# Performance work log

Hardware: AMD Instinct MI355X
Metric: run time of the kernel (lower is better)

The kernel has to match this reference:

```python
import jax, jax.numpy as jnp
import numpy as np

B, D, H, K = 8192, 1280, 16384, 64


def setup_inputs() -> dict:
    key = jax.random.key(0)
    k1, k2, k3 = jax.random.split(key, 3)
    x = jax.random.normal(k1, (B, D), dtype=jnp.float32)
    # encoder weight [hidden_dim, input_dim] (torch Linear layout)
    W_enc = jax.random.normal(k2, (H, D), dtype=jnp.float32) * (1.0 / np.sqrt(D))
    b_enc = jnp.zeros((H,), dtype=jnp.float32)
    # decoder weight [input_dim, hidden_dim], unit-norm columns scaled by 0.1
    W_dec = jax.random.normal(k3, (D, H), dtype=jnp.float32)
    W_dec = 0.1 * W_dec / jnp.linalg.norm(W_dec, axis=0, keepdims=True)
    b_dec = jnp.zeros((D,), dtype=jnp.float32)
    b_pre = jnp.zeros((D,), dtype=jnp.float32)
    return {"x": x, "W_enc": W_enc, "b_enc": b_enc, "W_dec": W_dec,
            "b_dec": b_dec, "b_pre": b_pre, "k": K}


def reference(x, W_enc, b_enc, W_dec, b_dec, b_pre, k):
    # --- encode ---
    x_centered = x - b_pre                                   # [B, D]
    pre = jnp.einsum('bd,hd->bh', x_centered, W_enc) + b_enc  # [B, H]
    vals, idx = jax.lax.top_k(pre, k)                        # [B, k]
    rows = jnp.arange(pre.shape[0])[:, None]                 # [B, 1]
    hidden = jnp.zeros_like(pre).at[rows, idx].set(jax.nn.relu(vals))  # [B, H]
    # --- decode ---
    reconstructed = jnp.einsum('bh,dh->bd', hidden, W_dec) + b_dec + b_pre
    # --- losses ---
    reconstruction_loss = jnp.mean((reconstructed - x) ** 2)
    l0 = jnp.mean(jnp.sum((hidden > 0).astype(jnp.float32), axis=-1))
    sparsity_loss = jnp.array(0.0, dtype=jnp.float32)
    loss = reconstruction_loss
    return reconstructed, hidden, loss, reconstruction_loss, sparsity_loss, l0
```

## Files before the change

### kernel.cpp

```cpp
#include <hip/hip_runtime.h>
#include <hip/hip_bf16.h>

constexpr int K_MAX    = 128;
constexpr int S_MAX    = 128;
constexpr int A_MAX    = 256;
constexpr int CAND_MAX = 512;
constexpr int BM = 128, BN = 128, BKF = 16;
constexpr int NBITER = 42;
constexpr int D_MAX   = 2048;
constexpr int H_FIX   = 16384;

typedef __attribute__((ext_vector_type(8))) short bf16x8;
typedef __attribute__((ext_vector_type(8))) unsigned short u16x8;
typedef __attribute__((ext_vector_type(4))) float f32x4;

__device__ inline unsigned short f2bf(float f) {
  unsigned u = __float_as_uint(f);
  return (unsigned short)((u + 0x7fff + ((u >> 16) & 1)) >> 16);
}
__device__ inline unsigned short key_of(float f) {
  unsigned short b = f2bf(f);
  return b ^ ((b & 0x8000) ? 0xFFFF : 0x8000);
}
__device__ inline float val_of_key(unsigned short kk) {
  unsigned short b = (kk & 0x8000) ? (unsigned short)(kk ^ 0x8000)
                                   : (unsigned short)(kk ^ 0xFFFF);
  return __uint_as_float(((unsigned)b) << 16);
}
__device__ inline float bf2f(unsigned short b) {
  return __uint_as_float(((unsigned)b) << 16);
}

__device__ inline int lds_slot(int r, int c) {
  return ((r >> 1) << 4) | ((r & 1) << 3) | (c ^ ((r >> 1) & 7));
}

__global__ __launch_bounds__(256) void prep_xb(
    const float* __restrict__ x, const float* __restrict__ b_pre,
    unsigned short* __restrict__ Xb, int D, size_t total4)
{
  for (size_t i = blockIdx.x * 256 + threadIdx.x; i < total4; i += (size_t)gridDim.x * 256) {
    const size_t e = i * 4;
    const int d = (int)(e % D);
    float4 xv = *reinterpret_cast<const float4*>(x + e);
    float4 bp = *reinterpret_cast<const float4*>(b_pre + d);
    ushort4 o;
    o.x = f2bf(xv.x - bp.x); o.y = f2bf(xv.y - bp.y);
    o.z = f2bf(xv.z - bp.z); o.w = f2bf(xv.w - bp.w);
    *reinterpret_cast<ushort4*>(Xb + e) = o;
  }
}

__global__ __launch_bounds__(256) void prep_wb(
    const float* __restrict__ W, unsigned short* __restrict__ Wb, size_t total4)
{
  for (size_t i = blockIdx.x * 256 + threadIdx.x; i < total4; i += (size_t)gridDim.x * 256) {
    const size_t e = i * 4;
    float4 wv = *reinterpret_cast<const float4*>(W + e);
    ushort4 o;
    o.x = f2bf(wv.x); o.y = f2bf(wv.y); o.z = f2bf(wv.z); o.w = f2bf(wv.w);
    *reinterpret_cast<ushort4*>(Wb + e) = o;
  }
}

__global__ __launch_bounds__(256) void enc_gemm_bf16(
    const unsigned short* __restrict__ Xb, const unsigned short* __restrict__ Wb,
    const float* __restrict__ b_enc, float* __restrict__ pre, int D, int H)
{
  __shared__ unsigned short As[2][128 * 64];
  __shared__ unsigned short Bs[2][128 * 64];
  const int tid  = threadIdx.x;
  const int wave = tid >> 6, lane = tid & 63;

  int lin = blockIdx.y * gridDim.x + blockIdx.x;
  const int nwg = gridDim.x * gridDim.y;
  if ((nwg & 7) == 0) {
    const int cpx = nwg >> 3;
    lin = (lin & 7) * cpx + (lin >> 3);
  }
  const int m0 = (lin / gridDim.x) * 128, n0 = (lin % gridDim.x) * 128;

  const int wm = (wave >> 1) * 64, wn = (wave & 1) * 64;
  const int l16 = lane & 15, lhi = lane >> 4;

  f32x4 acc[4][4];
#pragma unroll
  for (int i = 0; i < 4; ++i)
#pragma unroll
    for (int j = 0; j < 4; ++j) acc[i][j] = (f32x4){0.f, 0.f, 0.f, 0.f};

  const int NT = D / 64;

#pragma unroll
  for (int i = 0; i < 4; ++i) {
    const int base = wave * 64 + i * 256;
    const int idx  = base + lane;
    const int sr = idx >> 4, u = idx & 15;
    const int row = (sr << 1) | (u >> 3);
    const int ch  = (u & 7) ^ (sr & 7);
    __builtin_amdgcn_global_load_lds(
        (const __attribute__((address_space(1))) unsigned int*)(Xb + (size_t)(m0 + row) * D + ch * 8),
        (__attribute__((address_space(3))) unsigned int*)(As[0] + (size_t)base * 8), 16, 0, 0);
    __builtin_amdgcn_global_load_lds(
        (const __attribute__((address_space(1))) unsigned int*)(Wb + (size_t)(n0 + row) * D + ch * 8),
        (__attribute__((address_space(3))) unsigned int*)(Bs[0] + (size_t)base * 8), 16, 0, 0);
  }
  __syncthreads();

  int cur = 0;
  for (int t = 0; t < NT; ++t) {
    if (t + 1 < NT) {
      const int kb = (t + 1) * 64;
      const int nxt = cur ^ 1;
#pragma unroll
      for (int i = 0; i < 4; ++i) {
        const int base = wave * 64 + i * 256;
        const int idx  = base + lane;
        const int sr = idx >> 4, u = idx & 15;
        const int row = (sr << 1) | (u >> 3);
        const int ch  = (u & 7) ^ (sr & 7);
        __builtin_amdgcn_global_load_lds(
            (const __attribute__((address_space(1))) unsigned int*)(Xb + (size_t)(m0 + row) * D + kb + ch * 8),
            (__attribute__((address_space(3))) unsigned int*)(As[nxt] + (size_t)base * 8), 16, 0, 0);
        __builtin_amdgcn_global_load_lds(
            (const __attribute__((address_space(1))) unsigned int*)(Wb + (size_t)(n0 + row) * D + kb + ch * 8),
            (__attribute__((address_space(3))) unsigned int*)(Bs[nxt] + (size_t)base * 8), 16, 0, 0);
      }
    }
#pragma unroll
    for (int kk = 0; kk < 2; ++kk) {
      bf16x8 af[4], bfr[4];
#pragma unroll
      for (int mi = 0; mi < 4; ++mi)
        af[mi] = *reinterpret_cast<const bf16x8*>(
            As[cur] + (size_t)lds_slot(wm + mi * 16 + l16, kk * 4 + lhi) * 8);
#pragma unroll
      for (int ni = 0; ni < 4; ++ni)
        bfr[ni] = *reinterpret_cast<const bf16x8*>(
            Bs[cur] + (size_t)lds_slot(wn + ni * 16 + l16, kk * 4 + lhi) * 8);
#pragma unroll
      for (int mi = 0; mi < 4; ++mi)
#pragma unroll
        for (int ni = 0; ni < 4; ++ni)
          acc[mi][ni] = __builtin_amdgcn_mfma_f32_16x16x32_bf16(af[mi], bfr[ni], acc[mi][ni], 0, 0, 0);
    }
    __syncthreads();
    cur ^= 1;
  }

#pragma unroll
  for (int ni = 0; ni < 4; ++ni) {
    const int n = n0 + wn + ni * 16 + l16;
    const float be = b_enc[n];
#pragma unroll
    for (int mi = 0; mi < 4; ++mi) {
      const int mbase = m0 + wm + mi * 16 + lhi * 4;
#pragma unroll
      for (int r = 0; r < 4; ++r) {
        unsigned short* prow = (unsigned short*)(pre + (size_t)(mbase + r) * H);
        prow[n] = key_of(acc[mi][ni][r] + be);
      }
    }
  }
}

__global__ __launch_bounds__(256) void topk_classify_keys(
    const float* __restrict__ hidden,
    int* __restrict__ sure_ix, float* __restrict__ sure_val, int* __restrict__ sure_cnt,
    int* __restrict__ amb_ix, int* __restrict__ amb_cnt,
    const int* __restrict__ kptr, float delta)
{
  constexpr int H = H_FIX, NC = H_FIX / (256 * 8);
  __shared__ int hist[4096];
  __shared__ int chunk[256];
  __shared__ int misc[8];

  const int tid = threadIdx.x, b = blockIdx.x;
  const int k = min(*kptr, K_MAX);
  const unsigned short* krow = (const unsigned short*)(hidden + (size_t)b * H);

  if (tid < 8) misc[tid] = 0;
  for (int i = tid; i < 4096; i += 256) hist[i] = 0;

  u16x8 kv[NC];
#pragma unroll
  for (int i = 0; i < NC; ++i)
    kv[i] = *reinterpret_cast<const u16x8*>(krow + ((size_t)i * 256 + tid) * 8);
  __syncthreads();

#pragma unroll
  for (int i = 0; i < NC; ++i)
#pragma unroll
    for (int j = 0; j < 8; ++j)
      atomicAdd(&hist[((unsigned)(unsigned short)kv[i][j]) >> 4], 1);
  __syncthreads();

  int csum = 0;
#pragma unroll
  for (int j = 0; j < 16; ++j) csum += hist[tid * 16 + j];
  chunk[tid] = csum;
  __syncthreads();
  int gt = 0;
  for (int j = tid + 1; j < 256; ++j) gt += chunk[j];
  {
    int run = gt;
#pragma unroll
    for (int j = 15; j >= 0; --j) {
      const int hc = hist[tid * 16 + j];
      if (run < k && k <= run + hc) { misc[0] = tid * 16 + j; misc[1] = run; }
      run += hc;
    }
  }
  __syncthreads();
  const int b1 = misc[0];
  if (tid < 16) chunk[tid] = 0;
  __syncthreads();
#pragma unroll
  for (int i = 0; i < NC; ++i)
#pragma unroll
    for (int j = 0; j < 8; ++j) {
      const unsigned kk = (unsigned)(unsigned short)kv[i][j];
      if ((int)(kk >> 4) == b1) atomicAdd(&chunk[kk & 15], 1);
    }
  __syncthreads();
  if (tid == 0) {
    int run = misc[1];
    int K16 = b1 << 4;
    for (int j = 15; j >= 0; --j) {
      const int c = chunk[j];
      if (run < k && k <= run + c) K16 = (b1 << 4) | j;
      run += c;
    }
    const float v_lo = val_of_key((unsigned short)K16);
    const float v_hi = val_of_key((unsigned short)min(K16 + 1, 65535));
    const float ulp = v_hi - v_lo;
    const float vs = v_hi + delta;
    const float va = v_lo - ulp - delta;
    int ks = key_of(vs); if (val_of_key((unsigned short)ks) > vs) --ks;
    int ka = key_of(va); if (val_of_key((unsigned short)ka) < va) ++ka;
    misc[2] = ks; misc[3] = ka;
  }
  __syncthreads();
  const unsigned ks = (unsigned)misc[2], ka = (unsigned)misc[3];

#pragma unroll
  for (int i = 0; i < NC; ++i)
#pragma unroll
    for (int j = 0; j < 8; ++j) {
      const unsigned kk = (unsigned)(unsigned short)kv[i][j];
      if (kk > ks) {
        const int p = atomicAdd(&misc[4], 1);
        if (p < S_MAX) {
          const int h = (i * 256 + tid) * 8 + j;
          sure_ix[(size_t)b * S_MAX + p] = h;
          sure_val[(size_t)b * S_MAX + p] = val_of_key((unsigned short)kk);
        }
      } else if (kk >= ka) {
        const int p = atomicAdd(&misc[5], 1);
        if (p < A_MAX) amb_ix[(size_t)b * A_MAX + p] = (i * 256 + tid) * 8 + j;
      }
    }
  __syncthreads();
  if (tid == 0) {
    sure_cnt[b] = min(misc[4], S_MAX);
    amb_cnt[b]  = min(misc[5], A_MAX);
  }
}

__global__ __launch_bounds__(256) void refine_f64(
    const float* __restrict__ X, const float* __restrict__ b_pre,
    const float* __restrict__ W, const float* __restrict__ b_enc,
    const int* __restrict__ amb_ix, const int* __restrict__ amb_cnt,
    double* __restrict__ amb_sv, int D)
{
  __shared__ float xr[D_MAX];
  const int tid = threadIdx.x, b = blockIdx.x;
  const int C = min(amb_cnt[b], A_MAX);
  for (int d = tid; d < D; d += 256) xr[d] = X[(size_t)b * D + d] - b_pre[d];
  __syncthreads();
  const int wid = tid >> 6, lane = tid & 63;
  for (int c = wid; c < C; c += 4) {
    const int h = amb_ix[(size_t)b * A_MAX + c];
    const float* wr = W + (size_t)h * D;
    double s0 = 0.0, s1 = 0.0;
    int i = lane;
    for (; i + 64 < D; i += 128) {
      s0 += (double)xr[i] * (double)wr[i];
      s1 += (double)xr[i + 64] * (double)wr[i + 64];
    }
    if (i < D) s0 += (double)xr[i] * (double)wr[i];
    double s = s0 + s1;
    for (int off = 32; off; off >>= 1) s += __shfl_xor(s, off);
    if (lane == 0) amb_sv[(size_t)b * A_MAX + c] = s + (double)b_enc[h];
  }
}

__global__ __launch_bounds__(256) void rank_scatter2(
    const int* __restrict__ sure_ix, const float* __restrict__ sure_val,
    const int* __restrict__ sure_cnt,
    const int* __restrict__ amb_ix, const double* __restrict__ amb_sv,
    const int* __restrict__ amb_cnt, const int* __restrict__ kptr,
    float* __restrict__ hidden, int* __restrict__ tk_idx, float* __restrict__ tk_val)
{
  constexpr int H = H_FIX;
  __shared__ double asv[A_MAX];
  __shared__ int    aix[A_MAX];
  const int tid = threadIdx.x, b = blockIdx.x;
  const int k = min(*kptr, K_MAX);
  const int S = min(min(sure_cnt[b], S_MAX), k);
  const int A = min(amb_cnt[b], A_MAX);
  float* hrow = hidden + (size_t)b * H;

  for (int c = tid; c < A; c += 256) {
    asv[c] = amb_sv[(size_t)b * A_MAX + c];
    aix[c] = amb_ix[(size_t)b * A_MAX + c];
  }
  const float4 z4 = {0.f, 0.f, 0.f, 0.f};
  for (int i = tid; i < (H >> 2); i += 256)
    reinterpret_cast<float4*>(hrow)[i] = z4;
  __syncthreads();

  for (int i = tid; i < S; i += 256) {
    const int h = sure_ix[(size_t)b * S_MAX + i];
    const float v = sure_val[(size_t)b * S_MAX + i];
    const float rv = (v > 0.f) ? v : 0.f;
    hrow[h] = rv;
    tk_idx[(size_t)b * K_MAX + i] = h;
    tk_val[(size_t)b * K_MAX + i] = rv;
  }
  const int m = k - S;
  for (int c = tid; c < A; c += 256) {
    const double v = asv[c];
    const int h = aix[c];
    int r = 0;
    for (int j = 0; j < A; ++j) {
      const double vj = asv[j];
      r += ((vj > v) || (vj == v && aix[j] < h)) ? 1 : 0;
    }
    if (r < m) {
      const float rv = (v > 0.0) ? (float)v : 0.f;
      hrow[h] = rv;
      tk_idx[(size_t)b * K_MAX + S + r] = h;
      tk_val[(size_t)b * K_MAX + S + r] = rv;
    }
  }
}

__global__ __launch_bounds__(256, 2) void topk_select(
    const float* __restrict__ X, const float* __restrict__ b_pre,
    const float* __restrict__ W, const float* __restrict__ b_enc,
    float* __restrict__ hidden, int* __restrict__ tk_idx, float* __restrict__ tk_val,
    const int* __restrict__ kptr, int D, float margin)
{
  constexpr int H = H_FIX, NC = H_FIX / (256 * 8);
  __shared__ double cand_sv[CAND_MAX];
  __shared__ float  xr[D_MAX];
  __shared__ int    cand_ix[CAND_MAX];
  __shared__ int    hist[4096];
  __shared__ int    chunk[256];
  __shared__ int    misc[8];

  const int tid = threadIdx.x, b = blockIdx.x;
  const int k = min(*kptr, K_MAX);
  float* hrow = hidden + (size_t)b * H;
  const unsigned short* krow = (const unsigned short*)hrow;

  if (tid < 8) misc[tid] = 0;
  for (int i = tid; i < 4096; i += 256) hist[i] = 0;
  for (int d = tid; d < D; d += 256) xr[d] = X[(size_t)b * D + d] - b_pre[d];

  u16x8 kv[NC];
#pragma unroll
  for (int i = 0; i < NC; ++i)
    kv[i] = *reinterpret_cast<const u16x8*>(krow + ((size_t)i * 256 + tid) * 8);
  __syncthreads();

#pragma unroll
  for (int i = 0; i < NC; ++i)
#pragma unroll
    for (int j = 0; j < 8; ++j)
      atomicAdd(&hist[((unsigned)(unsigned short)kv[i][j]) >> 4], 1);
  __syncthreads();

  int csum = 0;
#pragma unroll
  for (int j = 0; j < 16; ++j) csum += hist[tid * 16 + j];
  chunk[tid] = csum;
  __syncthreads();
  int gt = 0;
  for (int j = tid + 1; j < 256; ++j) gt += chunk[j];
  {
    int run = gt;
#pragma unroll
    for (int j = 15; j >= 0; --j) {
      const int hc = hist[tid * 16 + j];
      if (run < k && k <= run + hc) { misc[0] = tid * 16 + j; misc[1] = run; }
      run += hc;
    }
  }
  __syncthreads();
  const int b1 = misc[0];
  if (tid < 16) chunk[tid] = 0;
  __syncthreads();
#pragma unroll
  for (int i = 0; i < NC; ++i)
#pragma unroll
    for (int j = 0; j < 8; ++j) {
      const unsigned kk = (unsigned)(unsigned short)kv[i][j];
      if ((int)(kk >> 4) == b1) atomicAdd(&chunk[kk & 15], 1);
    }
  __syncthreads();
  if (tid == 0) {
    int run = misc[1];
    int K16 = b1 << 4;
    for (int j = 15; j >= 0; --j) {
      const int c = chunk[j];
      if (run < k && k <= run + c) K16 = (b1 << 4) | j;
      run += c;
    }
    const float vthr = val_of_key((unsigned short)K16) - margin;
    int kt = (int)key_of(vthr);
    if (kt > K16) kt = K16;
    misc[2] = kt;
  }
  __syncthreads();
  const unsigned kthr = (unsigned)misc[2];

#pragma unroll
  for (int i = 0; i < NC; ++i)
#pragma unroll
    for (int j = 0; j < 8; ++j) {
      if ((unsigned)(unsigned short)kv[i][j] >= kthr) {
        const int pos = atomicAdd(&misc[3], 1);
        if (pos < CAND_MAX) cand_ix[pos] = (i * 256 + tid) * 8 + j;
      }
    }
  __syncthreads();
  const int C = min(misc[3], CAND_MAX);

  const float4 z4 = {0.f, 0.f, 0.f, 0.f};
  for (int i = tid; i < (H >> 2); i += 256)
    reinterpret_cast<float4*>(hrow)[i] = z4;

  const int wid = tid >> 6, lane = tid & 63;
  for (int c = wid; c < C; c += 4) {
    const int h = cand_ix[c];
    const float* wr = W + (size_t)h * D;
    double s = 0.0;
    for (int i = lane; i < D; i += 64) s += (double)xr[i] * (double)wr[i];
    for (int off = 32; off; off >>= 1) s += __shfl_xor(s, off);
    if (lane == 0) cand_sv[c] = s + (double)b_enc[h];
  }
  __syncthreads();

  for (int c = tid; c < C; c += 256) {
    const double v = cand_sv[c];
    const int h = cand_ix[c];
    int r = 0;
    for (int j = 0; j < C; ++j) {
      const double vj = cand_sv[j];
      r += ((vj > v) || (vj == v && cand_ix[j] < h)) ? 1 : 0;
    }
    if (r < k) {
      const float rv = (v > 0.0) ? (float)v : 0.f;
      hrow[h] = rv;
      tk_idx[(size_t)b * K_MAX + r] = h;
      tk_val[(size_t)b * K_MAX + r] = rv;
    }
  }
}

__global__ __launch_bounds__(256) void enc_gemm_f32(
    const float* __restrict__ X, const float* __restrict__ W,
    const float* __restrict__ b_enc, const float* __restrict__ b_pre,
    float* __restrict__ pre, int D, int H)
{
  __shared__ float As[BKF][BM + 4];
  __shared__ float Bs[BKF][BN + 4];
  const int tid = threadIdx.x;
  const int m0 = blockIdx.y * BM;
  const int n0 = blockIdx.x * BN;
  const int tx = tid & 15, ty = tid >> 4;
  float acc[8][8];
#pragma unroll
  for (int i = 0; i < 8; ++i)
#pragma unroll
    for (int j = 0; j < 8; ++j) acc[i][j] = 0.f;

  for (int kb = 0; kb < D; kb += BKF) {
#pragma unroll
    for (int t = 0; t < 2; ++t) {
      const int f4i = tid + t * 256;
      const int row = f4i >> 2;
      const int kq  = (f4i & 3) << 2;
      float4 xv = *reinterpret_cast<const float4*>(X + (size_t)(m0 + row) * D + kb + kq);
      float4 bp = *reinterpret_cast<const float4*>(b_pre + kb + kq);
      As[kq + 0][row] = xv.x - bp.x; As[kq + 1][row] = xv.y - bp.y;
      As[kq + 2][row] = xv.z - bp.z; As[kq + 3][row] = xv.w - bp.w;
      float4 wv = *reinterpret_cast<const float4*>(W + (size_t)(n0 + row) * D + kb + kq);
      Bs[kq + 0][row] = wv.x; Bs[kq + 1][row] = wv.y;
      Bs[kq + 2][row] = wv.z; Bs[kq + 3][row] = wv.w;
    }
    __syncthreads();
#pragma unroll
    for (int kk = 0; kk < BKF; ++kk) {
      float4 a0 = *reinterpret_cast<const float4*>(&As[kk][ty * 8]);
      float4 a1 = *reinterpret_cast<const float4*>(&As[kk][ty * 8 + 4]);
      float4 b0 = *reinterpret_cast<const float4*>(&Bs[kk][tx * 8]);
      float4 b1 = *reinterpret_cast<const float4*>(&Bs[kk][tx * 8 + 4]);
      float av[8] = {a0.x, a0.y, a0.z, a0.w, a1.x, a1.y, a1.z, a1.w};
      float bv[8] = {b0.x, b0.y, b0.z, b0.w, b1.x, b1.y, b1.z, b1.w};
#pragma unroll
      for (int i = 0; i < 8; ++i)
#pragma unroll
        for (int j = 0; j < 8; ++j) acc[i][j] += av[i] * bv[j];
    }
    __syncthreads();
  }
#pragma unroll
  for (int i = 0; i < 8; ++i) {
    const size_t m = (size_t)(m0 + ty * 8 + i);
#pragma unroll
    for (int j = 0; j < 8; j += 4) {
      const int n = n0 + tx * 8 + j;
      float4 o;
      o.x = acc[i][j + 0] + b_enc[n + 0];
      o.y = acc[i][j + 1] + b_enc[n + 1];
      o.z = acc[i][j + 2] + b_enc[n + 2];
      o.w = acc[i][j + 3] + b_enc[n + 3];
      *reinterpret_cast<float4*>(pre + m * H + n) = o;
    }
  }
}

__global__ __launch_bounds__(256) void topk_refine(
    const float* __restrict__ X, const float* __restrict__ b_pre,
    const float* __restrict__ W, const float* __restrict__ b_enc,
    float* __restrict__ hidden, int* __restrict__ tk_idx, float* __restrict__ tk_val,
    const int* __restrict__ kptr, int D, int H, float margin)
{
  extern __shared__ char smem_raw[];
  double* cand_val = reinterpret_cast<double*>(smem_raw);
  float*  xr       = reinterpret_cast<float*>(cand_val + CAND_MAX);
  int*    cand_idx = reinterpret_cast<int*>(xr + D);
  int*    misc     = cand_idx + CAND_MAX;

  const int tid = threadIdx.x;
  const int b = blockIdx.x;
  const int k = min(*kptr, K_MAX);
  float* hrow = hidden + (size_t)b * H;

  for (int i = tid; i < NBITER + 2; i += 256) misc[i] = 0;
  for (int d = tid; d < D; d += 256) xr[d] = X[(size_t)b * D + d] - b_pre[d];

  float f[64];
#pragma unroll
  for (int i = 0; i < 16; ++i) {
    const int base = i * 1024 + tid * 4;
    float4 v = {-3e38f, -3e38f, -3e38f, -3e38f};
    if (base + 3 < H) v = *reinterpret_cast<const float4*>(hrow + base);
    f[4 * i + 0] = v.x; f[4 * i + 1] = v.y; f[4 * i + 2] = v.z; f[4 * i + 3] = v.w;
  }
  __syncthreads();

  float lo = -1e4f, hi = 1e4f;
  for (int it = 0; it < NBITER; ++it) {
    const float mid = 0.5f * (lo + hi);
    int cnt = 0;
#pragma unroll
    for (int j = 0; j < 64; ++j) cnt += (f[j] >= mid) ? 1 : 0;
    for (int off = 32; off; off >>= 1) cnt += __shfl_xor(cnt, off);
    if ((tid & 63) == 0) atomicAdd(&misc[it], cnt);
    __syncthreads();
    if (misc[it] >= k) lo = mid; else hi = mid;
  }

  const float thresh = lo - margin;
#pragma unroll
  for (int j = 0; j < 64; ++j) {
    if (f[j] >= thresh) {
      const int h = (j >> 2) * 1024 + tid * 4 + (j & 3);
      if (h < H) {
        int pos = atomicAdd(&misc[NBITER], 1);
        if (pos < CAND_MAX) cand_idx[pos] = h;
      }
    }
  }
  __syncthreads();
  const int C = min(misc[NBITER], CAND_MAX);

  const int wid = tid >> 6, lane = tid & 63;
  for (int c = wid; c < C; c += 4) {
    const int h = cand_idx[c];
    const float* wr = W + (size_t)h * D;
    double s = 0.0;
    for (int i = lane; i < D; i += 64) s += (double)xr[i] * (double)wr[i];
    for (int off = 32; off; off >>= 1) s += __shfl_xor(s, off);
    if (lane == 0) cand_val[c] = s + (double)b_enc[h];
  }
  __syncthreads();

  const float4 z4 = {0.f, 0.f, 0.f, 0.f};
  for (int i = tid; i < (H >> 2); i += 256)
    reinterpret_cast<float4*>(hrow)[i] = z4;
  __syncthreads();

  for (int c = tid; c < C; c += 256) {
    const double v = cand_val[c];
    const int h = cand_idx[c];
    int r = 0;
    for (int j = 0; j < C; ++j) {
      const double vj = cand_val[j];
      r += ((vj > v) || (vj == v && cand_idx[j] < h)) ? 1 : 0;
    }
    if (r < k) {
      const float rv = (v > 0.0) ? (float)v : 0.f;
      hrow[h] = rv;
      tk_idx[(size_t)b * K_MAX + r] = h;
      tk_val[(size_t)b * K_MAX + r] = rv;
    }
  }
}

__global__ __launch_bounds__(256) void transpose_wdec_bf16(
    const float* __restrict__ Wsrc, unsigned short* __restrict__ WT, int D, int H)
{
  __shared__ float tile[32][33];
  const int c  = threadIdx.x & 31;
  const int r0 = threadIdx.x >> 5;
  const int h0 = blockIdx.x * 32;
  const int d0 = blockIdx.y * 32;
#pragma unroll
  for (int r = r0; r < 32; r += 8) {
    const int d = d0 + r, h = h0 + c;
    if (d < D && h < H) tile[r][c] = Wsrc[(size_t)d * H + h];
  }
  __syncthreads();
#pragma unroll
  for (int r = r0; r < 32; r += 8) {
    const int h = h0 + r, d = d0 + c;
    if (h < H && d < D) WT[(size_t)h * D + d] = f2bf(tile[c][r]);
  }
}

__global__ __launch_bounds__(256) void decode_loss(
    const float* __restrict__ X, const float* __restrict__ b_pre,
    const float* __restrict__ b_dec, const float* __restrict__ Wfull,
    const unsigned short* __restrict__ WTb,
    const int* __restrict__ tk_idx, const float* __restrict__ tk_val,
    const int* __restrict__ kptr,
    float* __restrict__ recon, double* __restrict__ row_ssq,
    int D, int H, int useWT)
{
  __shared__ int   sidx[K_MAX];
  __shared__ float sval[K_MAX];
  __shared__ double sd[4];
  const int tid = threadIdx.x, b = blockIdx.x;
  const int k = min(*kptr, K_MAX);
  if (tid < k) {
    sidx[tid] = tk_idx[(size_t)b * K_MAX + tid];
    sval[tid] = tk_val[(size_t)b * K_MAX + tid];
  }
  __syncthreads();
  double ssq = 0.0;
  const int D4 = D >> 2;
  for (int dc = tid; dc < D4; dc += 256) {
    const int d = dc * 4;
    float4 bd = *reinterpret_cast<const float4*>(b_dec + d);
    float4 bp = *reinterpret_cast<const float4*>(b_pre + d);
    float4 a = {bd.x + bp.x, bd.y + bp.y, bd.z + bp.z, bd.w + bp.w};
    if (useWT) {
#pragma unroll 4
      for (int j = 0; j < k; ++j) {
        const ushort4 w = *reinterpret_cast<const ushort4*>(WTb + (size_t)sidx[j] * D + d);
        const float s = sval[j];
        a.x += s * bf2f(w.x); a.y += s * bf2f(w.y);
        a.z += s * bf2f(w.z); a.w += s * bf2f(w.w);
      }
    } else {
#pragma unroll 4
      for (int j = 0; j < k; ++j) {
        const float s = sval[j];
        const int h = sidx[j];
        a.x += s * Wfull[(size_t)(d + 0) * H + h];
        a.y += s * Wfull[(size_t)(d + 1) * H + h];
        a.z += s * Wfull[(size_t)(d + 2) * H + h];
        a.w += s * Wfull[(size_t)(d + 3) * H + h];
      }
    }
    *reinterpret_cast<float4*>(recon + (size_t)b * D + d) = a;
    float4 xv = *reinterpret_cast<const float4*>(X + (size_t)b * D + d);
    const double d0 = (double)a.x - (double)xv.x;
    const double d1 = (double)a.y - (double)xv.y;
    const double d2 = (double)a.z - (double)xv.z;
    const double d3 = (double)a.w - (double)xv.w;
    ssq += d0 * d0 + d1 * d1 + d2 * d2 + d3 * d3;
  }
  for (int off = 32; off; off >>= 1) ssq += __shfl_xor(ssq, off);
  if ((tid & 63) == 0) sd[tid >> 6] = ssq;
  __syncthreads();
  if (tid == 0) row_ssq[b] = sd[0] + sd[1] + sd[2] + sd[3];
}

__global__ __launch_bounds__(256) void finalize_part(
    const double* __restrict__ row_ssq, const float* __restrict__ tk_val,
    const int* __restrict__ kptr, double* __restrict__ part_s, int* __restrict__ part_c,
    int Bdim, int rows_per_blk)
{
  __shared__ double sd[4];
  __shared__ int si[4];
  const int tid = threadIdx.x;
  const int k = min(*kptr, K_MAX);
  const int b0 = blockIdx.x * rows_per_blk;
  const int b1 = min(b0 + rows_per_blk, Bdim);
  double s = 0.0;
  for (int i = b0 + tid; i < b1; i += 256) s += row_ssq[i];
  int cnt = 0;
  const int total = (b1 - b0) * k;
  for (int i = tid; i < total; i += 256) {
    const int bb = b0 + i / k, j = i - (i / k) * k;
    cnt += (tk_val[(size_t)bb * K_MAX + j] > 0.f) ? 1 : 0;
  }
  for (int off = 32; off; off >>= 1) { s += __shfl_xor(s, off); cnt += __shfl_xor(cnt, off); }
  if ((tid & 63) == 0) { sd[tid >> 6] = s; si[tid >> 6] = cnt; }
  __syncthreads();
  if (tid == 0) {
    part_s[blockIdx.x] = sd[0] + sd[1] + sd[2] + sd[3];
    part_c[blockIdx.x] = si[0] + si[1] + si[2] + si[3];
  }
}

__global__ __launch_bounds__(64) void finalize_k2(
    const double* __restrict__ part_s, const int* __restrict__ part_c,
    float* __restrict__ scalars, int nparts, int Bdim, int D)
{
  const int tid = threadIdx.x;
  double s = (tid < nparts) ? part_s[tid] : 0.0;
  int cnt = (tid < nparts) ? part_c[tid] : 0;
  for (int off = 32; off; off >>= 1) { s += __shfl_xor(s, off); cnt += __shfl_xor(cnt, off); }
  if (tid == 0) {
    const double rl = s / ((double)Bdim * (double)D);
    scalars[0] = (float)rl;
    scalars[1] = (float)rl;
    scalars[2] = 0.f;
    scalars[3] = (float)((double)cnt / Bdim);
  }
}

extern "C" void kernel_launch(void* const* d_in, const int* in_sizes, int n_in,
                              void* d_out, int out_size, void* d_ws, size_t ws_size,
                              hipStream_t stream)
{
  const float* x     = (const float*)d_in[0];
  const float* W_enc = (const float*)d_in[1];
  const float* b_enc = (const float*)d_in[2];
  const float* W_dec = (const float*)d_in[3];
  const float* b_dec = (const float*)d_in[4];
  const float* b_pre = (const float*)d_in[5];
  const int*   kptr  = (const int*)d_in[6];

  const int D = in_sizes[4];
  const int H = in_sizes[2];
  const int B = in_sizes[0] / D;

  float* recon   = (float*)d_out;
  float* hidden  = recon + (size_t)B * D;
  float* scalars = hidden + (size_t)B * H;

  size_t off = 0;
  int* tk_idx = (int*)((char*)d_ws + off);        off += (size_t)B * K_MAX * sizeof(int);
  float* tk_val = (float*)((char*)d_ws + off);    off += (size_t)B * K_MAX * sizeof(float);
  off = (off + 7) & ~(size_t)7;
  double* row_ssq = (double*)((char*)d_ws + off); off += (size_t)B * sizeof(double);
  double* part_s = (double*)((char*)d_ws + off);  off += 64 * sizeof(double);
  int* part_c = (int*)((char*)d_ws + off);        off += 64 * sizeof(int);
  off = (off + 7) & ~(size_t)7;

  unsigned short* Xb = (unsigned short*)((char*)d_ws + off);
  off += (size_t)B * D * sizeof(unsigned short);
  unsigned short* Wb = (unsigned short*)((char*)d_ws + off);
  off += (size_t)H * D * sizeof(unsigned short);
  const int useBF16 = (off <= ws_size) ? 1 : 0;

  unsigned short* WTb = (unsigned short*)((char*)d_ws + off);
  off += (size_t)D * H * sizeof(unsigned short);
  const int useWT = (off <= ws_size) ? 1 : 0;

  int* sure_ix = (int*)((char*)d_ws + off);       off += (size_t)B * S_MAX * sizeof(int);
  float* sure_val = (float*)((char*)d_ws + off);  off += (size_t)B * S_MAX * sizeof(float);
  int* sure_cnt = (int*)((char*)d_ws + off);      off += (size_t)B * sizeof(int);
  int* amb_ix = (int*)((char*)d_ws + off);        off += (size_t)B * A_MAX * sizeof(int);
  int* amb_cnt = (int*)((char*)d_ws + off);       off += (size_t)B * sizeof(int);
  off = (off + 7) & ~(size_t)7;
  double* amb_sv = (double*)((char*)d_ws + off);  off += (size_t)B * A_MAX * sizeof(double);
  const int useSPLIT = (useBF16 && off <= ws_size) ? 1 : 0;

  const bool fast_ok = (D % 64 == 0) && (D <= D_MAX) &&
                       (H == H_FIX) && (B % 128 == 0);

  if (useBF16 && fast_ok) {
    const size_t tx4 = (size_t)B * D / 4, tw4 = (size_t)H * D / 4;
    prep_xb<<<2048, 256, 0, stream>>>(x, b_pre, Xb, D, tx4);
    prep_wb<<<2048, 256, 0, stream>>>(W_enc, Wb, tw4);
    dim3 gg(H / 128, B / 128);
    enc_gemm_bf16<<<gg, 256, 0, stream>>>(Xb, Wb, b_enc, hidden, D, H);
    if (useSPLIT) {
      topk_classify_keys<<<B, 256, 0, stream>>>(hidden, sure_ix, sure_val, sure_cnt,
                                                amb_ix, amb_cnt, kptr, 0.05f);
      refine_f64<<<B, 256, 0, stream>>>(x, b_pre, W_enc, b_enc, amb_ix, amb_cnt, amb_sv, D);
      rank_scatter2<<<B, 256, 0, stream>>>(sure_ix, sure_val, sure_cnt,
                                           amb_ix, amb_sv, amb_cnt, kptr,
                                           hidden, tk_idx, tk_val);
    } else {
      topk_select<<<B, 256, 0, stream>>>(x, b_pre, W_enc, b_enc, hidden,
                                         tk_idx, tk_val, kptr, D, 0.04f);
    }
  } else {
    dim3 gg(H / BN, B / BM);
    enc_gemm_f32<<<gg, 256, 0, stream>>>(x, W_enc, b_enc, b_pre, hidden, D, H);
    const size_t sh = CAND_MAX * sizeof(double) + (size_t)D * sizeof(float)
                    + CAND_MAX * sizeof(int) + (NBITER + 8) * sizeof(int);
    topk_refine<<<B, 256, sh, stream>>>(x, b_pre, W_enc, b_enc, hidden,
                                        tk_idx, tk_val, kptr, D, H, 1e-3f);
  }

  if (useWT)
    transpose_wdec_bf16<<<dim3((H + 31) / 32, (D + 31) / 32), 256, 0, stream>>>(W_dec, WTb, D, H);

  decode_loss<<<B, 256, 0, stream>>>(x, b_pre, b_dec, W_dec, WTb,
                                     tk_idx, tk_val, kptr, recon, row_ssq, D, H, useWT);

  const int rpb = (B + 63) / 64;
  finalize_part<<<64, 256, 0, stream>>>(row_ssq, tk_val, kptr, part_s, part_c, B, rpb);
  finalize_k2<<<1, 64, 0, stream>>>(part_s, part_c, scalars, 64, B, D);
}
```

Before: 1.182 ms.

## Fuse f64 refine into rank-scatter, move row zeroing into classify, drop GEMM swizzle

Merges the double-precision refinement of ambiguous candidates into the rank/scatter kernel, so their refined scores stay in shared memory and the global amb_sv buffer and one kernel launch go away. Zeroing each hidden row moves into the top-k classify kernel, after the bf16 keys have been read into registers. The GEMM also drops its XCD-aware block-index remap and uses plain blockIdx mapping. Dropping the remap may reduce L2 reuse across chiplets, and the fused kernel carries more shared memory per block.

```diff
diff --git a/kernel.cpp b/kernel.cpp
--- a/kernel.cpp
+++ b/kernel.cpp
@@ -71,15 +71,7 @@
   __shared__ unsigned short Bs[2][128 * 64];
   const int tid  = threadIdx.x;
   const int wave = tid >> 6, lane = tid & 63;
-
-  int lin = blockIdx.y * gridDim.x + blockIdx.x;
-  const int nwg = gridDim.x * gridDim.y;
-  if ((nwg & 7) == 0) {
-    const int cpx = nwg >> 3;
-    lin = (lin & 7) * cpx + (lin >> 3);
-  }
-  const int m0 = (lin / gridDim.x) * 128, n0 = (lin % gridDim.x) * 128;
-
+  const int m0 = blockIdx.y * 128, n0 = blockIdx.x * 128;
   const int wm = (wave >> 1) * 64, wn = (wave & 1) * 64;
   const int l16 = lane & 15, lhi = lane >> 4;
 
@@ -165,7 +157,7 @@
 }
 
 __global__ __launch_bounds__(256) void topk_classify_keys(
-    const float* __restrict__ hidden,
+    float* __restrict__ hidden,
     int* __restrict__ sure_ix, float* __restrict__ sure_val, int* __restrict__ sure_cnt,
     int* __restrict__ amb_ix, int* __restrict__ amb_cnt,
     const int* __restrict__ kptr, float delta)
@@ -177,7 +169,8 @@
 
   const int tid = threadIdx.x, b = blockIdx.x;
   const int k = min(*kptr, K_MAX);
-  const unsigned short* krow = (const unsigned short*)(hidden + (size_t)b * H);
+  float* hrow = hidden + (size_t)b * H;
+  const unsigned short* krow = (const unsigned short*)hrow;
 
   if (tid < 8) misc[tid] = 0;
   for (int i = tid; i < 4096; i += 256) hist[i] = 0;
@@ -187,6 +180,10 @@
   for (int i = 0; i < NC; ++i)
     kv[i] = *reinterpret_cast<const u16x8*>(krow + ((size_t)i * 256 + tid) * 8);
   __syncthreads();
+
+  const float4 z4 = {0.f, 0.f, 0.f, 0.f};
+  for (int i = tid; i < (H >> 2); i += 256)
+    reinterpret_cast<float4*>(hrow)[i] = z4;
 
 #pragma unroll
   for (int i = 0; i < NC; ++i)
@@ -267,42 +264,17 @@
   }
 }
 
-__global__ __launch_bounds__(256) void refine_f64(
+__global__ __launch_bounds__(256) void refine_scatter(
     const float* __restrict__ X, const float* __restrict__ b_pre,
     const float* __restrict__ W, const float* __restrict__ b_enc,
-    const int* __restrict__ amb_ix, const int* __restrict__ amb_cnt,
-    double* __restrict__ amb_sv, int D)
-{
-  __shared__ float xr[D_MAX];
-  const int tid = threadIdx.x, b = blockIdx.x;
-  const int C = min(amb_cnt[b], A_MAX);
-  for (int d = tid; d < D; d += 256) xr[d] = X[(size_t)b * D + d] - b_pre[d];
-  __syncthreads();
-  const int wid = tid >> 6, lane = tid & 63;
-  for (int c = wid; c < C; c += 4) {
-    const int h = amb_ix[(size_t)b * A_MAX + c];
-    const float* wr = W + (size_t)h * D;
-    double s0 = 0.0, s1 = 0.0;
-    int i = lane;
-    for (; i + 64 < D; i += 128) {
-      s0 += (double)xr[i] * (double)wr[i];
-      s1 += (double)xr[i + 64] * (double)wr[i + 64];
-    }
-    if (i < D) s0 += (double)xr[i] * (double)wr[i];
-    double s = s0 + s1;
-    for (int off = 32; off; off >>= 1) s += __shfl_xor(s, off);
-    if (lane == 0) amb_sv[(size_t)b * A_MAX + c] = s + (double)b_enc[h];
-  }
-}
-
-__global__ __launch_bounds__(256) void rank_scatter2(
     const int* __restrict__ sure_ix, const float* __restrict__ sure_val,
     const int* __restrict__ sure_cnt,
-    const int* __restrict__ amb_ix, const double* __restrict__ amb_sv,
-    const int* __restrict__ amb_cnt, const int* __restrict__ kptr,
-    float* __restrict__ hidden, int* __restrict__ tk_idx, float* __restrict__ tk_val)
+    const int* __restrict__ amb_ix, const int* __restrict__ amb_cnt,
+    const int* __restrict__ kptr,
+    float* __restrict__ hidden, int* __restrict__ tk_idx, float* __restrict__ tk_val, int D)
 {
   constexpr int H = H_FIX;
+  __shared__ float  xr[D_MAX];
   __shared__ double asv[A_MAX];
   __shared__ int    aix[A_MAX];
   const int tid = threadIdx.x, b = blockIdx.x;
@@ -311,14 +283,8 @@
   const int A = min(amb_cnt[b], A_MAX);
   float* hrow = hidden + (size_t)b * H;
 
-  for (int c = tid; c < A; c += 256) {
-    asv[c] = amb_sv[(size_t)b * A_MAX + c];
-    aix[c] = amb_ix[(size_t)b * A_MAX + c];
-  }
-  const float4 z4 = {0.f, 0.f, 0.f, 0.f};
-  for (int i = tid; i < (H >> 2); i += 256)
-    reinterpret_cast<float4*>(hrow)[i] = z4;
-  __syncthreads();
+  for (int d = tid; d < D; d += 256) xr[d] = X[(size_t)b * D + d] - b_pre[d];
+  for (int c = tid; c < A; c += 256) aix[c] = amb_ix[(size_t)b * A_MAX + c];
 
   for (int i = tid; i < S; i += 256) {
     const int h = sure_ix[(size_t)b * S_MAX + i];
@@ -328,6 +294,25 @@
     tk_idx[(size_t)b * K_MAX + i] = h;
     tk_val[(size_t)b * K_MAX + i] = rv;
   }
+  __syncthreads();
+
+  const int wid = tid >> 6, lane = tid & 63;
+  for (int c = wid; c < A; c += 4) {
+    const int h = aix[c];
+    const float* wr = W + (size_t)h * D;
+    double s0 = 0.0, s1 = 0.0;
+    int i = lane;
+    for (; i + 64 < D; i += 128) {
+      s0 += (double)xr[i] * (double)wr[i];
+      s1 += (double)xr[i + 64] * (double)wr[i + 64];
+    }
+    if (i < D) s0 += (double)xr[i] * (double)wr[i];
+    double s = s0 + s1;
+    for (int off = 32; off; off >>= 1) s += __shfl_xor(s, off);
+    if (lane == 0) asv[c] = s + (double)b_enc[h];
+  }
+  __syncthreads();
+
   const int m = k - S;
   for (int c = tid; c < A; c += 256) {
     const double v = asv[c];
@@ -792,7 +777,6 @@
   int* amb_ix = (int*)((char*)d_ws + off);        off += (size_t)B * A_MAX * sizeof(int);
   int* amb_cnt = (int*)((char*)d_ws + off);       off += (size_t)B * sizeof(int);
   off = (off + 7) & ~(size_t)7;
-  double* amb_sv = (double*)((char*)d_ws + off);  off += (size_t)B * A_MAX * sizeof(double);
   const int useSPLIT = (useBF16 && off <= ws_size) ? 1 : 0;
 
   const bool fast_ok = (D % 64 == 0) && (D <= D_MAX) &&
@@ -807,10 +791,10 @@
     if (useSPLIT) {
       topk_classify_keys<<<B, 256, 0, stream>>>(hidden, sure_ix, sure_val, sure_cnt,
                                                 amb_ix, amb_cnt, kptr, 0.05f);
-      refine_f64<<<B, 256, 0, stream>>>(x, b_pre, W_enc, b_enc, amb_ix, amb_cnt, amb_sv, D);
-      rank_scatter2<<<B, 256, 0, stream>>>(sure_ix, sure_val, sure_cnt,
-                                           amb_ix, amb_sv, amb_cnt, kptr,
-                                           hidden, tk_idx, tk_val);
+      refine_scatter<<<B, 256, 0, stream>>>(x, b_pre, W_enc, b_enc,
+                                            sure_ix, sure_val, sure_cnt,
+                                            amb_ix, amb_cnt, kptr,
+                                            hidden, tk_idx, tk_val, D);
     } else {
       topk_select<<<B, 256, 0, stream>>>(x, b_pre, W_enc, b_enc, hidden,
                                          tk_idx, tk_val, kptr, D, 0.04f);
```

Result: faster. 1.136 ms (-3.9%).
